# Kernel optimization log

Measured on AMD Instinct MI355X. Metric: run time of the kernel, lower is better.

## Reference

```python
import jax, jax.numpy as jnp
import numpy as np

B, T, D = 8, 2048, 1024
DK, DV = 1024, 1024


def setup_inputs() -> dict:
    key = jax.random.key(0)
    ks = jax.random.split(key, 11)
    s = 0.02
    return {
        "query": jax.random.normal(ks[0], (B, T, D), jnp.float32),
        "keys": jax.random.normal(ks[1], (B, T, D), jnp.float32),
        "values": jax.random.normal(ks[2], (B, T, D), jnp.float32),
        "Wq": jax.random.normal(ks[3], (D, DK), jnp.float32) * s,
        "bq": jnp.zeros((DK,), jnp.float32),
        "Wk": jax.random.normal(ks[4], (D, DK), jnp.float32) * s,
        "bk": jnp.zeros((DK,), jnp.float32),
        "Wv": jax.random.normal(ks[5], (D, DV), jnp.float32) * s,
        "bv": jnp.zeros((DV,), jnp.float32),
        "Wo": jax.random.normal(ks[6], (DV, D), jnp.float32) * s,
        "bo": jnp.zeros((D,), jnp.float32),
        "apply_mask": 1,
    }


def reference(query, keys, values, Wq, bq, Wk, bk, Wv, bv, Wo, bo, apply_mask):
    # input projections
    q = query @ Wq + bq   # [B, T, DK]
    k = keys @ Wk + bk    # [B, T, DK]
    v = values @ Wv + bv  # [B, T, DV]
    dk = jnp.asarray(DK, jnp.float32)
    # explicit full score matrix, as in the original (non-flash) module
    scores = jnp.einsum("btd,bsd->bts", q, k) / jnp.sqrt(dk)  # [B, T, T]
    if apply_mask:
        Tq = q.shape[1]
        causal = jnp.triu(jnp.ones((Tq, Tq), bool), 1)  # True above diagonal
        scores = jnp.where(causal[None, :, :], -jnp.inf, scores)
    weights = jax.nn.softmax(scores, axis=-1)
    context = jnp.einsum("bts,bsd->btd", weights, v)  # [B, T, DV]
    return context @ Wo + bo  # [B, T, D]
```

## Files before the change

kernel.cpp:

```cpp
#include <hip/hip_runtime.h>
#include <hip/hip_bf16.h>


typedef __attribute__((ext_vector_type(8))) short bf16x8;
typedef __attribute__((ext_vector_type(4))) float f32x4;

#define DEVI __device__ __forceinline__
#define VM_GATE(n) asm volatile("s_waitcnt vmcnt(" #n ")" ::: "memory")
#define LGKM0()    asm volatile("s_waitcnt lgkmcnt(0)" ::: "memory")

DEVI unsigned short f2bf(float f) {
  union { float f; unsigned u; } v; v.f = f;
  unsigned r = v.u + 0x7FFFu + ((v.u >> 16) & 1u);
  return (unsigned short)(r >> 16);
}

DEVI unsigned pkbf(float a, float b) {
  unsigned r;
  asm("v_cvt_pk_bf16_f32 %0, %1, %2" : "=v"(r) : "v"(a), "v"(b));
  return r;
}

DEVI void load_lds16(const void* g, void* l) {
  __builtin_amdgcn_global_load_lds(
      (const __attribute__((address_space(1))) unsigned int*)g,
      (__attribute__((address_space(3))) unsigned int*)l,
      16, 0, 0);
}

constexpr int BM = 256, BN = 256, BK = 64;

DEVI void stage_chunk(char* chunk, const unsigned short* src, long ldx,
                      int kbase, int tid) {
#pragma unroll
  for (int i = 0; i < 2; ++i) {
    int tloc = i * 512 + tid;
    int r = tloc >> 2, ps = tloc & 3;
    int q = (ps - (r >> 1)) & 3;
    load_lds16(src + (size_t)r * ldx + kbase + q * 8,
               chunk + (i * 512 + (tid & 0x1C0)) * 16);
  }
}

DEVI void stage_chunk_h(char* chunk, const unsigned short* src, long ldx,
                        int kbase, int tid) {
  int r = tid >> 2, ps = tid & 3;
  int q = (ps - (r >> 1)) & 3;
  load_lds16(src + (size_t)r * ldx + kbase + q * 8,
             chunk + (tid & 0x1C0) * 16);
}

DEVI bf16x8 frag(const char* chunk, int r, int q0) {
  int sp = (q0 + (r >> 1)) & 3;
  return *(const bf16x8*)(chunk + r * 64 + sp * 16);
}

DEVI void a32_load(float4* fr, const float* src, long lda, int kbase, int tid) {
#pragma unroll
  for (int j = 0; j < 4; ++j) {
    int cell = j * 512 + tid;
    int r = cell >> 3, q = cell & 7;
    const float* p = src + (size_t)r * lda + kbase + q * 8;
    fr[2 * j]     = *(const float4*)p;
    fr[2 * j + 1] = *(const float4*)(p + 4);
  }
}
DEVI void a32_write(char* chunk0, char* chunk1, const float4* fr, int tid) {
#pragma unroll
  for (int j = 0; j < 4; ++j) {
    int cell = j * 512 + tid;
    int r = cell >> 3, q = cell & 7;
    int kh = q >> 2, qq = q & 3;
    int sp = (qq + (r >> 1)) & 3;
    uint4 u;
    u.x = pkbf(fr[2 * j].x,     fr[2 * j].y);
    u.y = pkbf(fr[2 * j].z,     fr[2 * j].w);
    u.z = pkbf(fr[2 * j + 1].x, fr[2 * j + 1].y);
    u.w = pkbf(fr[2 * j + 1].z, fr[2 * j + 1].w);
    *(uint4*)((kh ? chunk1 : chunk0) + r * 64 + sp * 16) = u;
  }
}

DEVI void swz_bid(int nx, int ny, int nz, int& bx, int& by, int& z) {
  int bid = (blockIdx.z * ny + blockIdx.y) * nx + blockIdx.x;
  const int nwg = nx * ny * nz;
  if ((nwg & 7) == 0) bid = (bid & 7) * (nwg >> 3) + (bid >> 3);
  bx = bid % nx;
  int t1 = bid / nx;
  by = t1 % ny;
  z  = t1 / ny;
}

template<bool A_F32, bool OUT_F32, bool OUT_TRANS, bool DO_BIAS, bool DO_SCALE,
         bool DO_CSKIP, bool DO_KCLAMP>
__global__ __launch_bounds__(512, 2) void gemm_k(
    const void* __restrict__ Ap, long lda, long sAz,
    const unsigned short* __restrict__ Bt, long ldb, long sBz,
    void* __restrict__ Cp, long ldc, long sCz,
    const float* __restrict__ bias, float scale,
    const int* __restrict__ maskp, int Kdim)
{
  int bx, by, z;
  swz_bid(gridDim.x, gridDim.y, gridDim.z, bx, by, z);

  const int n0 = bx * BN;
  const int m0 = by * BM;
  if constexpr (DO_CSKIP) {
    if (maskp[0] && n0 > m0 + (BM - 1)) return;
  }
  int Keff = Kdim;
  if constexpr (DO_KCLAMP) {
    if (maskp[0]) Keff = min(Kdim, m0 + BM);
  }

  __shared__ alignas(16) char LDSb[2][2][2][16384];

  const int tid  = threadIdx.x;
  const int lane = tid & 63;
  const int w    = tid >> 6;
  const int wr   = w >> 2, wc = w & 3;
  const int la   = lane & 15;
  const int q0   = lane >> 4;

  f32x4 acc[8][4];
  const f32x4 z4 = {0.f, 0.f, 0.f, 0.f};
#pragma unroll
  for (int mi = 0; mi < 8; ++mi)
#pragma unroll
    for (int ni = 0; ni < 4; ++ni) acc[mi][ni] = z4;

  const unsigned short* Ag0 = (const unsigned short*)Ap + (size_t)z * sAz + (size_t)m0 * lda;
  const float*          Af0 = (const float*)Ap + (size_t)z * sAz + (size_t)m0 * lda;
  const unsigned short* Bg0 = Bt + (size_t)z * sBz + (size_t)n0 * ldb;

  const int nt = Keff / BK;
  float4 fr[8];

  if constexpr (A_F32) {
    a32_load(fr, Af0, lda, 0, tid);
    stage_chunk((char*)LDSb[0][1][0], Bg0, ldb, 0,  tid);
    stage_chunk((char*)LDSb[0][1][1], Bg0, ldb, 32, tid);
    VM_GATE(4);
    a32_write((char*)LDSb[0][0][0], (char*)LDSb[0][0][1], fr, tid);
    if (nt > 1) a32_load(fr, Af0, lda, BK, tid);
    LGKM0();
  } else {
    stage_chunk((char*)LDSb[0][0][0], Ag0, lda, 0,  tid);
    stage_chunk((char*)LDSb[0][1][0], Bg0, ldb, 0,  tid);
    stage_chunk((char*)LDSb[0][0][1], Ag0, lda, 32, tid);
    stage_chunk((char*)LDSb[0][1][1], Bg0, ldb, 32, tid);
  }

  for (int t = 0; t < nt; ++t) {
    const int buf = t & 1, nb = buf ^ 1;
    const bool pf = (t + 1 < nt);
    const int kb = (t + 1) * BK;
    const char* Ak0 = LDSb[buf][0][0];
    const char* Bk0 = LDSb[buf][1][0];
    const char* Ak1 = LDSb[buf][0][1];
    const char* Bk1 = LDSb[buf][1][1];
    bf16x8 bfv[4], af[8];

    if constexpr (A_F32) {
      if (pf) { VM_GATE(10); } else { VM_GATE(2); }
    } else {
      VM_GATE(4);
    }
    __builtin_amdgcn_s_barrier();
    __builtin_amdgcn_sched_barrier(0);
#pragma unroll
    for (int ni = 0; ni < 4; ++ni) bfv[ni] = frag(Bk0, wc * 64 + ni * 16 + la, q0);
#pragma unroll
    for (int mi = 0; mi < 8; ++mi) af[mi] = frag(Ak0, wr * 128 + mi * 16 + la, q0);
    if (pf) {
      if constexpr (!A_F32) stage_chunk((char*)LDSb[nb][0][0], Ag0, lda, kb, tid);
      stage_chunk((char*)LDSb[nb][1][0], Bg0, ldb, kb, tid);
    }
    __builtin_amdgcn_s_setprio(1);
#pragma unroll
    for (int mi = 0; mi < 8; ++mi)
#pragma unroll
      for (int ni = 0; ni < 4; ++ni)
        acc[mi][ni] = __builtin_amdgcn_mfma_f32_16x16x32_bf16(af[mi], bfv[ni], acc[mi][ni], 0, 0, 0);
    __builtin_amdgcn_s_setprio(0);

    if constexpr (A_F32) {
      if (pf) { VM_GATE(10); } else { VM_GATE(0); }
    } else {
      if (pf) { VM_GATE(4); } else { VM_GATE(0); }
    }
    __builtin_amdgcn_s_barrier();
    __builtin_amdgcn_sched_barrier(0);
#pragma unroll
    for (int ni = 0; ni < 4; ++ni) bfv[ni] = frag(Bk1, wc * 64 + ni * 16 + la, q0);
#pragma unroll
    for (int mi = 0; mi < 8; ++mi) af[mi] = frag(Ak1, wr * 128 + mi * 16 + la, q0);
    if (pf) {
      if constexpr (!A_F32) stage_chunk((char*)LDSb[nb][0][1], Ag0, lda, kb + 32, tid);
      stage_chunk((char*)LDSb[nb][1][1], Bg0, ldb, kb + 32, tid);
      if constexpr (A_F32) {
        VM_GATE(4);
        a32_write((char*)LDSb[nb][0][0], (char*)LDSb[nb][0][1], fr, tid);
        if (t + 2 < nt) a32_load(fr, Af0, lda, kb + BK, tid);
      }
    }
    __builtin_amdgcn_s_setprio(1);
#pragma unroll
    for (int mi = 0; mi < 8; ++mi)
#pragma unroll
      for (int ni = 0; ni < 4; ++ni)
        acc[mi][ni] = __builtin_amdgcn_mfma_f32_16x16x32_bf16(af[mi], bfv[ni], acc[mi][ni], 0, 0, 0);
    __builtin_amdgcn_s_setprio(0);
    if constexpr (A_F32) {
      if (pf) { LGKM0(); __builtin_amdgcn_sched_barrier(0); }
    }
  }

#pragma unroll
  for (int ni = 0; ni < 4; ++ni) {
    const int n = n0 + wc * 64 + ni * 16 + la;
    float bv = 0.f;
    if constexpr (DO_BIAS) bv = bias[n];
#pragma unroll
    for (int mi = 0; mi < 8; ++mi) {
      const int m = m0 + wr * 128 + mi * 16 + (q0 << 2);
      f32x4 c = acc[mi][ni];
      if constexpr (DO_SCALE) c = c * scale;
      if constexpr (DO_BIAS)  c = c + bv;
      if constexpr (OUT_TRANS) {
        unsigned short* C = (unsigned short*)Cp + (size_t)z * sCz + (size_t)n * ldc + m;
        ushort4 h;
        h.x = f2bf(c[0]); h.y = f2bf(c[1]); h.z = f2bf(c[2]); h.w = f2bf(c[3]);
        *(ushort4*)C = h;
      } else if constexpr (OUT_F32) {
        float* C = (float*)Cp + (size_t)z * sCz + (size_t)m * ldc + n;
#pragma unroll
        for (int j = 0; j < 4; ++j) C[(size_t)j * ldc] = c[j];
      } else {
        unsigned short* C = (unsigned short*)Cp + (size_t)z * sCz + (size_t)m * ldc + n;
#pragma unroll
        for (int j = 0; j < 4; ++j) C[(size_t)j * ldc] = f2bf(c[j]);
      }
    }
  }
}

template<bool OUT_F32, bool DO_BIAS, bool DO_SCALE, bool DO_CSKIP, bool DO_KCLAMP>
__global__ __launch_bounds__(512, 4) void gemm_s(
    const unsigned short* __restrict__ Ab, long lda, long sAz,
    const unsigned short* __restrict__ Bt, long ldb, long sBz,
    void* __restrict__ Cp, long ldc, long sCz,
    const float* __restrict__ bias, float scale,
    const int* __restrict__ maskp, int Kdim)
{
  int bx, by, z;
  swz_bid(gridDim.x, gridDim.y, gridDim.z, bx, by, z);

  const int n0 = bx * 128;
  const int m0 = by * 256;
  if constexpr (DO_CSKIP) {
    if (maskp[0] && n0 > m0 + 255) return;
  }
  int Keff = Kdim;
  if constexpr (DO_KCLAMP) {
    if (maskp[0]) Keff = min(Kdim, m0 + 256);
  }

  __shared__ alignas(16) char LA[2][16384];
  __shared__ alignas(16) char LB[2][8192];

  const int tid  = threadIdx.x;
  const int lane = tid & 63;
  const int w    = tid >> 6;
  const int wr   = w >> 1, wc = w & 1;
  const int la   = lane & 15;
  const int q0   = lane >> 4;

  f32x4 acc[4][4];
  const f32x4 z4 = {0.f, 0.f, 0.f, 0.f};
#pragma unroll
  for (int mi = 0; mi < 4; ++mi)
#pragma unroll
    for (int ni = 0; ni < 4; ++ni) acc[mi][ni] = z4;

  const unsigned short* Ag0 = Ab + (size_t)z * sAz + (size_t)m0 * lda;
  const unsigned short* Bg0 = Bt + (size_t)z * sBz + (size_t)n0 * ldb;

  stage_chunk((char*)LA[0], Ag0, lda, 0, tid);
  stage_chunk_h((char*)LB[0], Bg0, ldb, 0, tid);

  const int nt = Keff / 32;
  for (int t = 0; t < nt; ++t) {
    const int buf = t & 1;
    const bool pf = (t + 1 < nt);
    VM_GATE(0);
    __builtin_amdgcn_s_barrier();
    __builtin_amdgcn_sched_barrier(0);
    bf16x8 af[4], bfv[4];
#pragma unroll
    for (int mi = 0; mi < 4; ++mi) af[mi] = frag((char*)LA[buf], wr * 64 + mi * 16 + la, q0);
#pragma unroll
    for (int ni = 0; ni < 4; ++ni) bfv[ni] = frag((char*)LB[buf], wc * 64 + ni * 16 + la, q0);
    if (pf) {
      stage_chunk((char*)LA[buf ^ 1], Ag0, lda, (t + 1) * 32, tid);
      stage_chunk_h((char*)LB[buf ^ 1], Bg0, ldb, (t + 1) * 32, tid);
    }
    __builtin_amdgcn_s_setprio(1);
#pragma unroll
    for (int mi = 0; mi < 4; ++mi)
#pragma unroll
      for (int ni = 0; ni < 4; ++ni)
        acc[mi][ni] = __builtin_amdgcn_mfma_f32_16x16x32_bf16(af[mi], bfv[ni], acc[mi][ni], 0, 0, 0);
    __builtin_amdgcn_s_setprio(0);
  }

#pragma unroll
  for (int ni = 0; ni < 4; ++ni) {
    const int n = n0 + wc * 64 + ni * 16 + la;
    float bv = 0.f;
    if constexpr (DO_BIAS) bv = bias[n];
#pragma unroll
    for (int mi = 0; mi < 4; ++mi) {
      const int m = m0 + wr * 64 + mi * 16 + (q0 << 2);
      f32x4 c = acc[mi][ni];
      if constexpr (DO_SCALE) c = c * scale;
      if constexpr (DO_BIAS)  c = c + bv;
      if constexpr (OUT_F32) {
        float* C = (float*)Cp + (size_t)z * sCz + (size_t)m * ldc + n;
#pragma unroll
        for (int j = 0; j < 4; ++j) C[(size_t)j * ldc] = c[j];
      } else {
        unsigned short* C = (unsigned short*)Cp + (size_t)z * sCz + (size_t)m * ldc + n;
#pragma unroll
        for (int j = 0; j < 4; ++j) C[(size_t)j * ldc] = f2bf(c[j]);
      }
    }
  }
}

__global__ __launch_bounds__(256) void wtrans_k(
    const float* __restrict__ W0, const float* __restrict__ W1,
    const float* __restrict__ W2, const float* __restrict__ W3,
    unsigned short* __restrict__ T0, unsigned short* __restrict__ T1,
    unsigned short* __restrict__ T2, unsigned short* __restrict__ T3)
{
  const float* W = blockIdx.z == 0 ? W0 : blockIdx.z == 1 ? W1
                 : blockIdx.z == 2 ? W2 : W3;
  unsigned short* Wt = blockIdx.z == 0 ? T0 : blockIdx.z == 1 ? T1
                     : blockIdx.z == 2 ? T2 : T3;
  __shared__ unsigned short L[64][80];
  const int n0 = blockIdx.x * 64, k0 = blockIdx.y * 64;
  const int tid = threadIdx.x;
#pragma unroll
  for (int p = 0; p < 4; ++p) {
    int idx = tid + p * 256;
    int r = idx >> 4, c4 = idx & 15;
    float4 v = *(const float4*)(W + (size_t)(k0 + r) * 1024 + n0 + c4 * 4);
    L[c4 * 4 + 0][r] = f2bf(v.x);
    L[c4 * 4 + 1][r] = f2bf(v.y);
    L[c4 * 4 + 2][r] = f2bf(v.z);
    L[c4 * 4 + 3][r] = f2bf(v.w);
  }
  __syncthreads();
#pragma unroll
  for (int p = 0; p < 2; ++p) {
    int idx = tid + p * 256;
    int n = idx >> 3, c8 = idx & 7;
    int4 v = *(const int4*)(&L[n][c8 * 8]);
    *(int4*)(Wt + (size_t)(n0 + n) * 1024 + k0 + c8 * 8) = v;
  }
}

__global__ __launch_bounds__(256) void softmax_k(
    const unsigned short* __restrict__ Sb, unsigned short* __restrict__ Pb,
    const int* __restrict__ maskp)
{
  const int row = blockIdx.x;
  const int t = row & 2047;
  const int msk = maskp[0];
  const int lim  = msk ? (t + 1) : 2048;
  const int wlim = msk ? ((t & ~255) + 256) : 2048;
  const unsigned short* Srow = Sb + (size_t)row * 2048;
  const int tid = threadIdx.x;
  const int cbase = tid * 8;

  float v[8];
  if (cbase < lim) {
    union { int4 q; unsigned short u[8]; } r;
    r.q = *(const int4*)(Srow + cbase);
#pragma unroll
    for (int j = 0; j < 8; ++j) {
      union { unsigned u; float f; } c;
      c.u = (unsigned)r.u[j] << 16;
      v[j] = c.f;
    }
#pragma unroll
    for (int j = 0; j < 8; ++j)
      if (cbase + j >= lim) v[j] = -__builtin_inff();
  } else {
#pragma unroll
    for (int j = 0; j < 8; ++j) v[j] = -__builtin_inff();
  }

  float mx = v[0];
#pragma unroll
  for (int j = 1; j < 8; ++j) mx = fmaxf(mx, v[j]);
#pragma unroll
  for (int off = 32; off; off >>= 1) mx = fmaxf(mx, __shfl_xor(mx, off, 64));

  __shared__ float redm[4], reds[4];
  const int wid = tid >> 6;
  if ((tid & 63) == 0) redm[wid] = mx;
  __syncthreads();
  mx = fmaxf(fmaxf(redm[0], redm[1]), fmaxf(redm[2], redm[3]));

  float e[8], s = 0.f;
#pragma unroll
  for (int j = 0; j < 8; ++j) { e[j] = __expf(v[j] - mx); s += e[j]; }
#pragma unroll
  for (int off = 32; off; off >>= 1) s += __shfl_xor(s, off, 64);
  if ((tid & 63) == 0) reds[wid] = s;
  __syncthreads();
  s = reds[0] + reds[1] + reds[2] + reds[3];
  const float inv = 1.0f / s;

  if (cbase < wlim) {
    unsigned pk[4];
#pragma unroll
    for (int q = 0; q < 4; ++q)
      pk[q] = (unsigned)f2bf(e[2 * q] * inv) | ((unsigned)f2bf(e[2 * q + 1] * inv) << 16);
    int4 o; o.x = (int)pk[0]; o.y = (int)pk[1]; o.z = (int)pk[2]; o.w = (int)pk[3];
    *(int4*)(Pb + (size_t)row * 2048 + cbase) = o;
  }
}

extern "C" void kernel_launch(void* const* d_in, const int* in_sizes, int n_in,
                              void* d_out, int out_size, void* d_ws, size_t ws_size,
                              hipStream_t stream)
{
  const float* query  = (const float*)d_in[0];
  const float* keys   = (const float*)d_in[1];
  const float* values = (const float*)d_in[2];
  const float* Wq = (const float*)d_in[3];
  const float* bq = (const float*)d_in[4];
  const float* Wk = (const float*)d_in[5];
  const float* bk = (const float*)d_in[6];
  const float* Wv = (const float*)d_in[7];
  const float* bv = (const float*)d_in[8];
  const float* Wo = (const float*)d_in[9];
  const float* bo = (const float*)d_in[10];
  const int* maskp = (const int*)d_in[11];
  float* out = (float*)d_out;

  char* ws = (char*)d_ws;
  const size_t MB = 1ull << 20;
  unsigned short* wt_q = (unsigned short*)(ws + 0 * MB);
  unsigned short* wt_k = (unsigned short*)(ws + 2 * MB);
  unsigned short* wt_v = (unsigned short*)(ws + 4 * MB);
  unsigned short* wt_o = (unsigned short*)(ws + 6 * MB);
  unsigned short* Qb   = (unsigned short*)(ws + 8 * MB);
  unsigned short* Kb   = (unsigned short*)(ws + 40 * MB);
  unsigned short* Vt   = (unsigned short*)(ws + 72 * MB);
  unsigned short* Sb   = (unsigned short*)(ws + 104 * MB);
  unsigned short* Pb   = (unsigned short*)(ws + 168 * MB);
  unsigned short* ctx  = Qb;

  const dim3 blk(512);
  const long sXT = 2048l * 1024;

  wtrans_k<<<dim3(16, 16, 4), dim3(256), 0, stream>>>(
      Wq, Wk, Wv, Wo, wt_q, wt_k, wt_v, wt_o);

  gemm_k<true, false, false, true, false, false, false><<<dim3(4, 8, 8), blk, 0, stream>>>(
      query, 1024, sXT, wt_q, 1024, 0, Qb, 1024, sXT, bq, 1.f, nullptr, 1024);
  gemm_k<true, false, false, true, false, false, false><<<dim3(4, 8, 8), blk, 0, stream>>>(
      keys, 1024, sXT, wt_k, 1024, 0, Kb, 1024, sXT, bk, 1.f, nullptr, 1024);
  gemm_k<true, false, true, true, false, false, false><<<dim3(4, 8, 8), blk, 0, stream>>>(
      values, 1024, sXT, wt_v, 1024, 0, Vt, 2048, 1024l * 2048, bv, 1.f, nullptr, 1024);

  gemm_s<false, false, true, true, false><<<dim3(16, 8, 8), blk, 0, stream>>>(
      Qb, 1024, sXT, Kb, 1024, sXT, Sb, 2048, 2048l * 2048, nullptr, 0.03125f, maskp, 1024);

  softmax_k<<<dim3(16384), dim3(256), 0, stream>>>(Sb, Pb, maskp);

  gemm_s<false, false, false, false, true><<<dim3(8, 8, 8), blk, 0, stream>>>(
      Pb, 2048, 2048l * 2048, Vt, 2048, 1024l * 2048,
      ctx, 1024, sXT, nullptr, 1.f, maskp, 2048);

  gemm_s<true, true, false, false, false><<<dim3(8, 8, 8), blk, 0, stream>>>(
      ctx, 1024, sXT, wt_o, 1024, 0, out, 1024, sXT, bo, 1.f, nullptr, 1024);
}
```

Measured before the change: 319.9 us.

## Replace 256x256 fp32-input projection GEMM with 256x128 tile, BK=32 kernel

The Q/K/V projection GEMMs switch from a 256x256 tile with K-step 64 and 2 blocks per CU to a new gemm_sf kernel with a 256x128 tile, K-step 32 and launch bounds allowing 4 blocks per CU. fp32 activations are converted to bf16 in registers and written to LDS, with a single-stage prefetch. The grid doubles, giving better CU fill and more waves for latency hiding, at the cost of lower arithmetic intensity per tile, since each fp32 A row is re-read by twice as many blocks.

```diff
diff --git a/kernel.cpp b/kernel.cpp
--- a/kernel.cpp
+++ b/kernel.cpp
@@ -27,8 +27,6 @@
       (__attribute__((address_space(3))) unsigned int*)l,
       16, 0, 0);
 }
-
-constexpr int BM = 256, BN = 256, BK = 64;
 
 DEVI void stage_chunk(char* chunk, const unsigned short* src, long ldx,
                       int kbase, int tid) {
@@ -55,29 +53,28 @@
   return *(const bf16x8*)(chunk + r * 64 + sp * 16);
 }
 
-DEVI void a32_load(float4* fr, const float* src, long lda, int kbase, int tid) {
-#pragma unroll
-  for (int j = 0; j < 4; ++j) {
+DEVI void a32h_load(float4* fr, const float* src, long lda, int kbase, int tid) {
+#pragma unroll
+  for (int j = 0; j < 2; ++j) {
     int cell = j * 512 + tid;
-    int r = cell >> 3, q = cell & 7;
+    int r = cell >> 2, q = cell & 3;
     const float* p = src + (size_t)r * lda + kbase + q * 8;
     fr[2 * j]     = *(const float4*)p;
     fr[2 * j + 1] = *(const float4*)(p + 4);
   }
 }
-DEVI void a32_write(char* chunk0, char* chunk1, const float4* fr, int tid) {
-#pragma unroll
-  for (int j = 0; j < 4; ++j) {
+DEVI void a32h_write(char* chunk, const float4* fr, int tid) {
+#pragma unroll
+  for (int j = 0; j < 2; ++j) {
     int cell = j * 512 + tid;
-    int r = cell >> 3, q = cell & 7;
-    int kh = q >> 2, qq = q & 3;
-    int sp = (qq + (r >> 1)) & 3;
+    int r = cell >> 2, q = cell & 3;
+    int sp = (q + (r >> 1)) & 3;
     uint4 u;
     u.x = pkbf(fr[2 * j].x,     fr[2 * j].y);
     u.y = pkbf(fr[2 * j].z,     fr[2 * j].w);
     u.z = pkbf(fr[2 * j + 1].x, fr[2 * j + 1].y);
     u.w = pkbf(fr[2 * j + 1].z, fr[2 * j + 1].w);
-    *(uint4*)((kh ? chunk1 : chunk0) + r * 64 + sp * 16) = u;
+    *(uint4*)(chunk + r * 64 + sp * 16) = u;
   }
 }
 
@@ -89,160 +86,6 @@
   int t1 = bid / nx;
   by = t1 % ny;
   z  = t1 / ny;
-}
-
-template<bool A_F32, bool OUT_F32, bool OUT_TRANS, bool DO_BIAS, bool DO_SCALE,
-         bool DO_CSKIP, bool DO_KCLAMP>
-__global__ __launch_bounds__(512, 2) void gemm_k(
-    const void* __restrict__ Ap, long lda, long sAz,
-    const unsigned short* __restrict__ Bt, long ldb, long sBz,
-    void* __restrict__ Cp, long ldc, long sCz,
-    const float* __restrict__ bias, float scale,
-    const int* __restrict__ maskp, int Kdim)
-{
-  int bx, by, z;
-  swz_bid(gridDim.x, gridDim.y, gridDim.z, bx, by, z);
-
-  const int n0 = bx * BN;
-  const int m0 = by * BM;
-  if constexpr (DO_CSKIP) {
-    if (maskp[0] && n0 > m0 + (BM - 1)) return;
-  }
-  int Keff = Kdim;
-  if constexpr (DO_KCLAMP) {
-    if (maskp[0]) Keff = min(Kdim, m0 + BM);
-  }
-
-  __shared__ alignas(16) char LDSb[2][2][2][16384];
-
-  const int tid  = threadIdx.x;
-  const int lane = tid & 63;
-  const int w    = tid >> 6;
-  const int wr   = w >> 2, wc = w & 3;
-  const int la   = lane & 15;
-  const int q0   = lane >> 4;
-
-  f32x4 acc[8][4];
-  const f32x4 z4 = {0.f, 0.f, 0.f, 0.f};
-#pragma unroll
-  for (int mi = 0; mi < 8; ++mi)
-#pragma unroll
-    for (int ni = 0; ni < 4; ++ni) acc[mi][ni] = z4;
-
-  const unsigned short* Ag0 = (const unsigned short*)Ap + (size_t)z * sAz + (size_t)m0 * lda;
-  const float*          Af0 = (const float*)Ap + (size_t)z * sAz + (size_t)m0 * lda;
-  const unsigned short* Bg0 = Bt + (size_t)z * sBz + (size_t)n0 * ldb;
-
-  const int nt = Keff / BK;
-  float4 fr[8];
-
-  if constexpr (A_F32) {
-    a32_load(fr, Af0, lda, 0, tid);
-    stage_chunk((char*)LDSb[0][1][0], Bg0, ldb, 0,  tid);
-    stage_chunk((char*)LDSb[0][1][1], Bg0, ldb, 32, tid);
-    VM_GATE(4);
-    a32_write((char*)LDSb[0][0][0], (char*)LDSb[0][0][1], fr, tid);
-    if (nt > 1) a32_load(fr, Af0, lda, BK, tid);
-    LGKM0();
-  } else {
-    stage_chunk((char*)LDSb[0][0][0], Ag0, lda, 0,  tid);
-    stage_chunk((char*)LDSb[0][1][0], Bg0, ldb, 0,  tid);
-    stage_chunk((char*)LDSb[0][0][1], Ag0, lda, 32, tid);
-    stage_chunk((char*)LDSb[0][1][1], Bg0, ldb, 32, tid);
-  }
-
-  for (int t = 0; t < nt; ++t) {
-    const int buf = t & 1, nb = buf ^ 1;
-    const bool pf = (t + 1 < nt);
-    const int kb = (t + 1) * BK;
-    const char* Ak0 = LDSb[buf][0][0];
-    const char* Bk0 = LDSb[buf][1][0];
-    const char* Ak1 = LDSb[buf][0][1];
-    const char* Bk1 = LDSb[buf][1][1];
-    bf16x8 bfv[4], af[8];
-
-    if constexpr (A_F32) {
-      if (pf) { VM_GATE(10); } else { VM_GATE(2); }
-    } else {
-      VM_GATE(4);
-    }
-    __builtin_amdgcn_s_barrier();
-    __builtin_amdgcn_sched_barrier(0);
-#pragma unroll
-    for (int ni = 0; ni < 4; ++ni) bfv[ni] = frag(Bk0, wc * 64 + ni * 16 + la, q0);
-#pragma unroll
-    for (int mi = 0; mi < 8; ++mi) af[mi] = frag(Ak0, wr * 128 + mi * 16 + la, q0);
-    if (pf) {
-      if constexpr (!A_F32) stage_chunk((char*)LDSb[nb][0][0], Ag0, lda, kb, tid);
-      stage_chunk((char*)LDSb[nb][1][0], Bg0, ldb, kb, tid);
-    }
-    __builtin_amdgcn_s_setprio(1);
-#pragma unroll
-    for (int mi = 0; mi < 8; ++mi)
-#pragma unroll
-      for (int ni = 0; ni < 4; ++ni)
-        acc[mi][ni] = __builtin_amdgcn_mfma_f32_16x16x32_bf16(af[mi], bfv[ni], acc[mi][ni], 0, 0, 0);
-    __builtin_amdgcn_s_setprio(0);
-
-    if constexpr (A_F32) {
-      if (pf) { VM_GATE(10); } else { VM_GATE(0); }
-    } else {
-      if (pf) { VM_GATE(4); } else { VM_GATE(0); }
-    }
-    __builtin_amdgcn_s_barrier();
-    __builtin_amdgcn_sched_barrier(0);
-#pragma unroll
-    for (int ni = 0; ni < 4; ++ni) bfv[ni] = frag(Bk1, wc * 64 + ni * 16 + la, q0);
-#pragma unroll
-    for (int mi = 0; mi < 8; ++mi) af[mi] = frag(Ak1, wr * 128 + mi * 16 + la, q0);
-    if (pf) {
-      if constexpr (!A_F32) stage_chunk((char*)LDSb[nb][0][1], Ag0, lda, kb + 32, tid);
-      stage_chunk((char*)LDSb[nb][1][1], Bg0, ldb, kb + 32, tid);
-      if constexpr (A_F32) {
-        VM_GATE(4);
-        a32_write((char*)LDSb[nb][0][0], (char*)LDSb[nb][0][1], fr, tid);
-        if (t + 2 < nt) a32_load(fr, Af0, lda, kb + BK, tid);
-      }
-    }
-    __builtin_amdgcn_s_setprio(1);
-#pragma unroll
-    for (int mi = 0; mi < 8; ++mi)
-#pragma unroll
-      for (int ni = 0; ni < 4; ++ni)
-        acc[mi][ni] = __builtin_amdgcn_mfma_f32_16x16x32_bf16(af[mi], bfv[ni], acc[mi][ni], 0, 0, 0);
-    __builtin_amdgcn_s_setprio(0);
-    if constexpr (A_F32) {
-      if (pf) { LGKM0(); __builtin_amdgcn_sched_barrier(0); }
-    }
-  }
-
-#pragma unroll
-  for (int ni = 0; ni < 4; ++ni) {
-    const int n = n0 + wc * 64 + ni * 16 + la;
-    float bv = 0.f;
-    if constexpr (DO_BIAS) bv = bias[n];
-#pragma unroll
-    for (int mi = 0; mi < 8; ++mi) {
-      const int m = m0 + wr * 128 + mi * 16 + (q0 << 2);
-      f32x4 c = acc[mi][ni];
-      if constexpr (DO_SCALE) c = c * scale;
-      if constexpr (DO_BIAS)  c = c + bv;
-      if constexpr (OUT_TRANS) {
-        unsigned short* C = (unsigned short*)Cp + (size_t)z * sCz + (size_t)n * ldc + m;
-        ushort4 h;
-        h.x = f2bf(c[0]); h.y = f2bf(c[1]); h.z = f2bf(c[2]); h.w = f2bf(c[3]);
-        *(ushort4*)C = h;
-      } else if constexpr (OUT_F32) {
-        float* C = (float*)Cp + (size_t)z * sCz + (size_t)m * ldc + n;
-#pragma unroll
-        for (int j = 0; j < 4; ++j) C[(size_t)j * ldc] = c[j];
-      } else {
-        unsigned short* C = (unsigned short*)Cp + (size_t)z * sCz + (size_t)m * ldc + n;
-#pragma unroll
-        for (int j = 0; j < 4; ++j) C[(size_t)j * ldc] = f2bf(c[j]);
-      }
-    }
-  }
 }
 
 template<bool OUT_F32, bool DO_BIAS, bool DO_SCALE, bool DO_CSKIP, bool DO_KCLAMP>
@@ -329,6 +172,99 @@
         float* C = (float*)Cp + (size_t)z * sCz + (size_t)m * ldc + n;
 #pragma unroll
         for (int j = 0; j < 4; ++j) C[(size_t)j * ldc] = c[j];
+      } else {
+        unsigned short* C = (unsigned short*)Cp + (size_t)z * sCz + (size_t)m * ldc + n;
+#pragma unroll
+        for (int j = 0; j < 4; ++j) C[(size_t)j * ldc] = f2bf(c[j]);
+      }
+    }
+  }
+}
+
+template<bool OUT_TRANS, bool DO_BIAS>
+__global__ __launch_bounds__(512, 4) void gemm_sf(
+    const float* __restrict__ Af, long lda, long sAz,
+    const unsigned short* __restrict__ Bt, long ldb, long sBz,
+    void* __restrict__ Cp, long ldc, long sCz,
+    const float* __restrict__ bias, int Kdim)
+{
+  int bx, by, z;
+  swz_bid(gridDim.x, gridDim.y, gridDim.z, bx, by, z);
+
+  const int n0 = bx * 128;
+  const int m0 = by * 256;
+
+  __shared__ alignas(16) char LA[2][16384];
+  __shared__ alignas(16) char LB[2][8192];
+
+  const int tid  = threadIdx.x;
+  const int lane = tid & 63;
+  const int w    = tid >> 6;
+  const int wr   = w >> 1, wc = w & 1;
+  const int la   = lane & 15;
+  const int q0   = lane >> 4;
+
+  f32x4 acc[4][4];
+  const f32x4 z4 = {0.f, 0.f, 0.f, 0.f};
+#pragma unroll
+  for (int mi = 0; mi < 4; ++mi)
+#pragma unroll
+    for (int ni = 0; ni < 4; ++ni) acc[mi][ni] = z4;
+
+  const float*          Ag0 = Af + (size_t)z * sAz + (size_t)m0 * lda;
+  const unsigned short* Bg0 = Bt + (size_t)z * sBz + (size_t)n0 * ldb;
+
+  const int nt = Kdim / 32;
+  float4 fr[4];
+
+  a32h_load(fr, Ag0, lda, 0, tid);
+  stage_chunk_h((char*)LB[0], Bg0, ldb, 0, tid);
+  VM_GATE(1);
+  a32h_write((char*)LA[0], fr, tid);
+  if (nt > 1) a32h_load(fr, Ag0, lda, 32, tid);
+
+  for (int t = 0; t < nt; ++t) {
+    const int buf = t & 1, nb = buf ^ 1;
+    const bool pf = (t + 1 < nt);
+    if (pf) { VM_GATE(4); } else { VM_GATE(0); }
+    LGKM0();
+    __builtin_amdgcn_s_barrier();
+    __builtin_amdgcn_sched_barrier(0);
+    bf16x8 af[4], bfv[4];
+#pragma unroll
+    for (int mi = 0; mi < 4; ++mi) af[mi] = frag((char*)LA[buf], wr * 64 + mi * 16 + la, q0);
+#pragma unroll
+    for (int ni = 0; ni < 4; ++ni) bfv[ni] = frag((char*)LB[buf], wc * 64 + ni * 16 + la, q0);
+    if (pf) {
+      stage_chunk_h((char*)LB[nb], Bg0, ldb, (t + 1) * 32, tid);
+      VM_GATE(1);
+      a32h_write((char*)LA[nb], fr, tid);
+      if (t + 2 < nt) a32h_load(fr, Ag0, lda, (t + 2) * 32, tid);
+    }
+    __builtin_amdgcn_s_setprio(1);
+#pragma unroll
+    for (int mi = 0; mi < 4; ++mi)
+#pragma unroll
+      for (int ni = 0; ni < 4; ++ni)
+        acc[mi][ni] = __builtin_amdgcn_mfma_f32_16x16x32_bf16(af[mi], bfv[ni], acc[mi][ni], 0, 0, 0);
+    __builtin_amdgcn_s_setprio(0);
+  }
+
+#pragma unroll
+  for (int ni = 0; ni < 4; ++ni) {
+    const int n = n0 + wc * 64 + ni * 16 + la;
+    float bv = 0.f;
+    if constexpr (DO_BIAS) bv = bias[n];
+#pragma unroll
+    for (int mi = 0; mi < 4; ++mi) {
+      const int m = m0 + wr * 64 + mi * 16 + (q0 << 2);
+      f32x4 c = acc[mi][ni];
+      if constexpr (DO_BIAS) c = c + bv;
+      if constexpr (OUT_TRANS) {
+        unsigned short* C = (unsigned short*)Cp + (size_t)z * sCz + (size_t)n * ldc + m;
+        ushort4 h;
+        h.x = f2bf(c[0]); h.y = f2bf(c[1]); h.z = f2bf(c[2]); h.w = f2bf(c[3]);
+        *(ushort4*)C = h;
       } else {
         unsigned short* C = (unsigned short*)Cp + (size_t)z * sCz + (size_t)m * ldc + n;
 #pragma unroll
@@ -471,12 +407,12 @@
   wtrans_k<<<dim3(16, 16, 4), dim3(256), 0, stream>>>(
       Wq, Wk, Wv, Wo, wt_q, wt_k, wt_v, wt_o);
 
-  gemm_k<true, false, false, true, false, false, false><<<dim3(4, 8, 8), blk, 0, stream>>>(
-      query, 1024, sXT, wt_q, 1024, 0, Qb, 1024, sXT, bq, 1.f, nullptr, 1024);
-  gemm_k<true, false, false, true, false, false, false><<<dim3(4, 8, 8), blk, 0, stream>>>(
-      keys, 1024, sXT, wt_k, 1024, 0, Kb, 1024, sXT, bk, 1.f, nullptr, 1024);
-  gemm_k<true, false, true, true, false, false, false><<<dim3(4, 8, 8), blk, 0, stream>>>(
-      values, 1024, sXT, wt_v, 1024, 0, Vt, 2048, 1024l * 2048, bv, 1.f, nullptr, 1024);
+  gemm_sf<false, true><<<dim3(8, 8, 8), blk, 0, stream>>>(
+      query, 1024, sXT, wt_q, 1024, 0, Qb, 1024, sXT, bq, 1024);
+  gemm_sf<false, true><<<dim3(8, 8, 8), blk, 0, stream>>>(
+      keys, 1024, sXT, wt_k, 1024, 0, Kb, 1024, sXT, bk, 1024);
+  gemm_sf<true, true><<<dim3(8, 8, 8), blk, 0, stream>>>(
+      values, 1024, sXT, wt_v, 1024, 0, Vt, 2048, 1024l * 2048, bv, 1024);
 
   gemm_s<false, false, true, true, false><<<dim3(16, 8, 8), blk, 0, stream>>>(
       Qb, 1024, sXT, Kb, 1024, sXT, Sb, 2048, 2048l * 2048, nullptr, 0.03125f, maskp, 1024);
```

New measurement: 461.5 us. 44.3% more time.
